# Performance work log

Hardware: AMD Instinct MI355X
Metric: run time of the kernel (lower is better)

The kernel has to match this reference:

```python
import jax, jax.numpy as jnp
import numpy as np

HIDDEN = 2304
HEADS = 16
THETA = 10000.0
LN_EPS = 1e-5


def setup_inputs() -> dict:
    key = jax.random.key(0)
    ks = jax.random.split(key, 6)
    d = HIDDEN
    init = lambda k, shape: jax.random.normal(k, shape, jnp.float32) * 0.02
    return {
        "x": jax.random.normal(ks[0], (4, 2048, d), jnp.float32),
        "wq": init(ks[1], (d, d)), "bq": jnp.zeros((d,), jnp.float32),
        "wk": init(ks[2], (d, d)), "bk": jnp.zeros((d,), jnp.float32),
        "wv": init(ks[3], (d, d)), "bv": jnp.zeros((d,), jnp.float32),
        "wo": init(ks[4], (d, d)), "bo": jnp.zeros((d,), jnp.float32),
        "ln_g": jnp.ones((d,), jnp.float32),
        "ln_b": jnp.zeros((d,), jnp.float32),
    }


def reference(x, wq, bq, wk, bk, wv, bv, wo, bo, ln_g, ln_b):
    b, s, d = x.shape
    H = HEADS
    Dh = d // H

    # qkv projections (nn.Linear: x @ W^T + b)
    q = jnp.einsum('bsd,ed->bse', x, wq) + bq
    k = jnp.einsum('bsd,ed->bse', x, wk) + bk
    v = jnp.einsum('bsd,ed->bse', x, wv) + bv

    # RoPE over the FULL hidden dim (d/2 pairs), as in the source
    pos = jnp.arange(s, dtype=jnp.float32)                    # (s,)
    scale = jnp.arange(0, d, 2, dtype=jnp.float32) / d        # (d/2,)
    omega = 1.0 / (THETA ** scale)                            # (d/2,)
    ang = pos[:, None] * omega[None, :]                       # (s, d/2)
    cos, sin = jnp.cos(ang), jnp.sin(ang)

    def rot(t):
        t2 = t.reshape(b, s, d // 2, 2)
        x0, x1 = t2[..., 0], t2[..., 1]
        return jnp.stack([cos * x0 - sin * x1, sin * x0 + cos * x1], axis=-1).reshape(b, s, d)

    q, k = rot(q), rot(k)

    # split heads -> (b, H, s, Dh)
    q = q.reshape(b, s, H, Dh).transpose(0, 2, 1, 3)
    k = k.reshape(b, s, H, Dh).transpose(0, 2, 1, 3)
    v = v.reshape(b, s, H, Dh).transpose(0, 2, 1, 3)

    # NOTE: faithful to source: einsum labels make this HEAD-mixing
    # attention at each position: logits shape (b, H, s, H)
    att_scale = 1.0 / (Dh ** 0.5)
    logits = jnp.einsum('bnhd,bmhd->bnhm', q, k) * att_scale
    w = jax.nn.softmax(logits, axis=-1)                       # (b,H,s,H)
    out = jnp.einsum('bnhm,bmhd->bnhd', w, v)                 # (b,H,s,Dh)

    out = out.transpose(0, 2, 1, 3).reshape(b, s, d)
    out = jnp.einsum('bsd,ed->bse', out, wo) + bo

    # residual + LayerNorm (dropout in eval mode -> identity)
    y = x + out
    mu = jnp.mean(y, axis=-1, keepdims=True)
    var = jnp.mean((y - mu) ** 2, axis=-1, keepdims=True)
    return (y - mu) * jax.lax.rsqrt(var + LN_EPS) * ln_g + ln_b
```

## Files before the change

### kernel.cpp

```cpp
#include <hip/hip_runtime.h>
#include <stdint.h>
#include <stddef.h>

#define D_HID 2304
#define NTOK  8192
#define NQKV  6912
#define WELEMS 5308416
#define SEQ_MASK 2047

typedef unsigned short u16;
typedef __bf16 bf16x8 __attribute__((ext_vector_type(8)));
typedef float  f32x16 __attribute__((ext_vector_type(16)));
typedef float  f32x4  __attribute__((ext_vector_type(4)));

__device__ __forceinline__ u16 f2bf(float f) {
    unsigned int u = __builtin_bit_cast(unsigned int, f);
    u += 0x7fffu + ((u >> 16) & 1u);
    return (u16)(u >> 16);
}
__device__ __forceinline__ float bf2f(u16 h) {
    unsigned int u = ((unsigned int)h) << 16;
    return __builtin_bit_cast(float, u);
}

__device__ __forceinline__ void gl2lds16(const void* g, void* l) {
    __builtin_amdgcn_global_load_lds(
        (const __attribute__((address_space(1))) void*)g,
        (__attribute__((address_space(3))) void*)l,
        16, 0, 0);
}

__global__ __launch_bounds__(256) void cvt_f32_bf16(
    const float* __restrict__ src, u16* __restrict__ dst)
{
    size_t i = ((size_t)blockIdx.x * 256 + threadIdx.x) * 4;
    float4 f = *(const float4*)(src + i);
    ushort4 o = make_ushort4(f2bf(f.x), f2bf(f.y), f2bf(f.z), f2bf(f.w));
    *(ushort4*)(dst + i) = o;
}

__global__ __launch_bounds__(256) void cvt_weights(
    const float* __restrict__ wq, const float* __restrict__ wk,
    const float* __restrict__ wv, const float* __restrict__ wo,
    u16* __restrict__ dst,
    const float* __restrict__ bq, const float* __restrict__ bk,
    const float* __restrict__ bv, float* __restrict__ bqkv)
{
    int i = blockIdx.x * 256 + threadIdx.x;
    if (i < NQKV)
        bqkv[i] = (i < 2304) ? bq[i] : (i < 4608) ? bk[i - 2304] : bv[i - 4608];
    size_t base = (size_t)i * 4;
    int r = (int)(base / WELEMS);
    const float* src = (r == 0) ? wq : (r == 1) ? wk : (r == 2) ? wv : wo;
    float4 f = *(const float4*)(src + (base - (size_t)r * WELEMS));
    ushort4 o = make_ushort4(f2bf(f.x), f2bf(f.y), f2bf(f.z), f2bf(f.w));
    *(ushort4*)(dst + base) = o;
}

__global__ __launch_bounds__(512, 2) void gemm256_bt(
    const u16* __restrict__ A, const u16* __restrict__ B,
    const float* __restrict__ bias, u16* __restrict__ Cout,
    int M, int N, int K)
{
    __shared__ __align__(16) u16 lds2[65536];

    const int tid  = threadIdx.x;
    const int lane = tid & 63;
    const int wave = tid >> 6;
    const int NT   = K >> 6;
    (void)M;

    const int chunk = gridDim.x >> 3;
    const int bid = (blockIdx.x & 7) * chunk + (blockIdx.x >> 3);
    const int num_bn = N >> 8;
    const int bm = bid / num_bn;
    const int bn = bid - bm * num_bn;

    const int srow = lane >> 3;
    const u16* __restrict__ Ast = A + (size_t)(bm * 256 + wave * 8 + srow) * K
                                    + ((lane & 7) ^ srow) * 8;
    const u16* __restrict__ Bst = B + (size_t)(bn * 256 + wave * 8 + srow) * K
                                    + ((lane & 7) ^ srow) * 8;
    const size_t row64  = (size_t)64 * K;
    const size_t row128 = (size_t)128 * K;
    const int ldsW = wave * 512;

#define STAGE(buf, hsel, tt) do {                                              \
    const u16* g_ = ((hsel) < 2 ? Ast : Bst)                                   \
                    + (((hsel) & 1) ? row128 : 0) + (size_t)(tt) * 64;         \
    u16* l_ = lds2 + (buf) * 32768 + (((hsel) < 2) ? 0 : 16384)                \
              + (((hsel) & 1) ? 8192 : 0) + ldsW;                              \
    gl2lds16(g_, l_);                                                          \
    gl2lds16(g_ + row64, l_ + 4096);                                           \
} while (0)

    const int l15 = lane & 15, l4 = lane >> 4;
    const int aBase = (wave >> 2) * 8192 + l15 * 64;
    const int bBase = 16384 + ((wave >> 1) & 1) * 8192
                      + ((wave & 1) * 64 + l15) * 64;
    const int s0 = ((l4    ) ^ (lane & 7)) * 8;
    const int s1 = ((l4 + 4) ^ (lane & 7)) * 8;

    f32x4 acc[8][4] = {};
    bf16x8 Bk0[4], Bk1[4], Aev[4], Aod[4];

    STAGE(0, 2, 0); STAGE(0, 3, 0); STAGE(0, 0, 0); STAGE(0, 1, 0);
    STAGE(1, 2, 1); STAGE(1, 3, 1); STAGE(1, 0, 1);
    asm volatile("s_waitcnt vmcnt(6)" ::: "memory");
    __builtin_amdgcn_s_barrier();
#pragma unroll
    for (int n = 0; n < 4; ++n)
        Bk0[n] = *(const bf16x8*)(lds2 + bBase + n * 1024 + s0);
#pragma unroll
    for (int mo = 0; mo < 4; ++mo)
        Aev[mo] = *(const bf16x8*)(lds2 + aBase + mo * 1024 + s0);

    for (int t = 0; t < NT; ++t) {
        const int cur = t & 1;
        const u16* lc = lds2 + cur * 32768;
        const u16* ln = lds2 + (cur ^ 1) * 32768;
        const bool st1 = (t + 1 < NT);
        const bool st2 = (t + 2 < NT);

#pragma unroll
        for (int n = 0; n < 4; ++n)
            Bk1[n] = *(const bf16x8*)(lc + bBase + n * 1024 + s1);
#pragma unroll
        for (int mo = 0; mo < 4; ++mo)
            Aod[mo] = *(const bf16x8*)(lc + aBase + (4 + mo) * 1024 + s0);
        if (st1) STAGE(cur ^ 1, 1, t + 1);
        __builtin_amdgcn_sched_barrier(0);
        __builtin_amdgcn_s_setprio(1);
#pragma unroll
        for (int mo = 0; mo < 4; ++mo)
#pragma unroll
            for (int n = 0; n < 4; ++n)
                acc[mo][n] = __builtin_amdgcn_mfma_f32_16x16x32_bf16(
                    Aev[mo], Bk0[n], acc[mo][n], 0, 0, 0);
        __builtin_amdgcn_s_setprio(0);
        __builtin_amdgcn_sched_barrier(0);
        __builtin_amdgcn_s_barrier();

#pragma unroll
        for (int mo = 0; mo < 4; ++mo)
            Aev[mo] = *(const bf16x8*)(lc + aBase + mo * 1024 + s1);
        if (st2) STAGE(cur, 2, t + 2);
        __builtin_amdgcn_sched_barrier(0);
        __builtin_amdgcn_s_setprio(1);
#pragma unroll
        for (int mo = 0; mo < 4; ++mo)
#pragma unroll
            for (int n = 0; n < 4; ++n)
                acc[4 + mo][n] = __builtin_amdgcn_mfma_f32_16x16x32_bf16(
                    Aod[mo], Bk0[n], acc[4 + mo][n], 0, 0, 0);
        __builtin_amdgcn_s_setprio(0);
        __builtin_amdgcn_sched_barrier(0);
        asm volatile("s_waitcnt lgkmcnt(0)" ::: "memory");
        __builtin_amdgcn_s_barrier();

#pragma unroll
        for (int mo = 0; mo < 4; ++mo)
            Aod[mo] = *(const bf16x8*)(lc + aBase + (4 + mo) * 1024 + s1);
        if (st2) STAGE(cur, 3, t + 2);
        if (st2)      asm volatile("s_waitcnt vmcnt(4)" ::: "memory");
        else if (st1) asm volatile("s_waitcnt vmcnt(0)" ::: "memory");
        if (st1) {
            __builtin_amdgcn_s_barrier();
#pragma unroll
            for (int n = 0; n < 4; ++n)
                Bk0[n] = *(const bf16x8*)(ln + bBase + n * 1024 + s0);
        }
        __builtin_amdgcn_sched_barrier(0);
        __builtin_amdgcn_s_setprio(1);
#pragma unroll
        for (int mo = 0; mo < 4; ++mo)
#pragma unroll
            for (int n = 0; n < 4; ++n)
                acc[mo][n] = __builtin_amdgcn_mfma_f32_16x16x32_bf16(
                    Aev[mo], Bk1[n], acc[mo][n], 0, 0, 0);
        __builtin_amdgcn_s_setprio(0);
        __builtin_amdgcn_sched_barrier(0);
        asm volatile("s_waitcnt lgkmcnt(0)" ::: "memory");
        __builtin_amdgcn_s_barrier();

        if (st2) STAGE(cur, 0, t + 2);
        if (st1) {
#pragma unroll
            for (int mo = 0; mo < 4; ++mo)
                Aev[mo] = *(const bf16x8*)(ln + aBase + mo * 1024 + s0);
        }
        __builtin_amdgcn_sched_barrier(0);
        __builtin_amdgcn_s_setprio(1);
#pragma unroll
        for (int mo = 0; mo < 4; ++mo)
#pragma unroll
            for (int n = 0; n < 4; ++n)
                acc[4 + mo][n] = __builtin_amdgcn_mfma_f32_16x16x32_bf16(
                    Aod[mo], Bk1[n], acc[4 + mo][n], 0, 0, 0);
        __builtin_amdgcn_s_setprio(0);
        __builtin_amdgcn_sched_barrier(0);
        asm volatile("s_waitcnt lgkmcnt(0)" ::: "memory");
        __builtin_amdgcn_s_barrier();
    }
#undef STAGE

    const int wm0 = (wave >> 2) * 128, wn0 = (wave & 3) * 64;
#pragma unroll
    for (int n = 0; n < 4; ++n) {
        const int gn = bn * 256 + wn0 + n * 16 + l15;
        const float bv = bias[gn];
#pragma unroll
        for (int m = 0; m < 8; ++m) {
            const int gm = bm * 256 + wm0 + m * 16 + l4 * 4;
#pragma unroll
            for (int j = 0; j < 4; ++j)
                Cout[(size_t)(gm + j) * N + gn] = f2bf(acc[m][n][j] + bv);
        }
    }
}

template<int MODE>
__global__ __launch_bounds__(256, 3) void gemm_bt(
    const u16* __restrict__ A, const u16* __restrict__ B,
    const float* __restrict__ bias, u16* __restrict__ Cout,
    const u16* __restrict__ resid, int M, int N, int K)
{
    __shared__ __align__(16) u16 As[128 * 64];
    __shared__ __align__(16) u16 Bs[128 * 64];

    const int tid  = threadIdx.x;
    const int lane = tid & 63;
    const int wave = tid >> 6;

    const int num_bn = N >> 7;
    const int rem = blockIdx.x % (num_bn << 3);
    const int bn  = rem >> 3;
    const int bm  = ((blockIdx.x / (num_bn << 3)) << 3) + (rem & 7);

    const int srow = tid >> 3;
    const int sc   = (tid & 7) ^ (srow & 7);
    const u16* Ag = A + (size_t)(bm * 128 + srow) * K + sc * 8;
    const u16* Bg = B + (size_t)(bn * 128 + srow) * K + sc * 8;
    const size_t row32 = (size_t)32 * K;
    u16* asd = As + wave * 512;
    u16* bsd = Bs + wave * 512;

    const int rl = lane & 31;
    const int h  = lane >> 5;
    const int swz = rl & 7;
    const int wm = (wave >> 1) * 64;
    const int wn = (wave & 1) * 64;

    f32x16 acc[2][2] = {};

    for (int kb = 0; kb < K; kb += 64) {
        __syncthreads();
#pragma unroll
        for (int r = 0; r < 4; ++r) {
            gl2lds16(Ag + kb + r * row32, asd + r * 2048);
            gl2lds16(Bg + kb + r * row32, bsd + r * 2048);
        }
        __syncthreads();

#pragma unroll
        for (int s = 0; s < 4; ++s) {
            const int ch = ((s * 2 + h) ^ swz) * 8;
            bf16x8 a0 = *(const bf16x8*)(As + (wm      + rl) * 64 + ch);
            bf16x8 a1 = *(const bf16x8*)(As + (wm + 32 + rl) * 64 + ch);
            bf16x8 b0 = *(const bf16x8*)(Bs + (wn      + rl) * 64 + ch);
            bf16x8 b1 = *(const bf16x8*)(Bs + (wn + 32 + rl) * 64 + ch);
            acc[0][0] = __builtin_amdgcn_mfma_f32_32x32x16_bf16(a0, b0, acc[0][0], 0, 0, 0);
            acc[0][1] = __builtin_amdgcn_mfma_f32_32x32x16_bf16(a0, b1, acc[0][1], 0, 0, 0);
            acc[1][0] = __builtin_amdgcn_mfma_f32_32x32x16_bf16(a1, b0, acc[1][0], 0, 0, 0);
            acc[1][1] = __builtin_amdgcn_mfma_f32_32x32x16_bf16(a1, b1, acc[1][1], 0, 0, 0);
        }
    }

#pragma unroll
    for (int mt = 0; mt < 2; ++mt) {
#pragma unroll
        for (int nt = 0; nt < 2; ++nt) {
            const int gn = bn * 128 + wn + nt * 32 + rl;
            const float bv = bias[gn];
#pragma unroll
            for (int reg = 0; reg < 16; ++reg) {
                const int gm = bm * 128 + wm + mt * 32 +
                               (reg & 3) + 8 * (reg >> 2) + 4 * h;
                const size_t idx = (size_t)gm * N + gn;
                float v = acc[mt][nt][reg] + bv;
                if constexpr (MODE == 1) v += bf2f(resid[idx]);
                Cout[idx] = f2bf(v);
            }
        }
    }
}

#define HROW 148
__global__ __launch_bounds__(256) void attn_headmix(
    const u16* __restrict__ QKV, u16* __restrict__ Aout)
{
    __shared__ __align__(16) float qs[16 * HROW];
    __shared__ __align__(16) float ks[16 * HROW];
    __shared__ __align__(16) float vs[16 * HROW];
    __shared__ __align__(16) float wsmT[256];

    const int tid = threadIdx.x;
    const int t   = blockIdx.x;
    const float fpos = (float)(t & SEQ_MASK);
    const u16* row = QKV + (size_t)t * NQKV;

    const float OMEGA_C = -2.0f * 13.287712379549449f / 2304.0f;
    const float INV2PI  = 0.15915494309189535f;

    for (int c = tid; c < 864; c += 256) {
        uint4 raw = *(const uint4*)(row + c * 8);
        float f[8];
        f[0] = bf2f(raw.x & 0xffff); f[1] = bf2f(raw.x >> 16);
        f[2] = bf2f(raw.y & 0xffff); f[3] = bf2f(raw.y >> 16);
        f[4] = bf2f(raw.z & 0xffff); f[5] = bf2f(raw.z >> 16);
        f[6] = bf2f(raw.w & 0xffff); f[7] = bf2f(raw.w >> 16);
        if (c < 576) {
            const int cc = (c < 288) ? c : c - 288;
            const int p0 = cc * 4;
#pragma unroll
            for (int jp = 0; jp < 4; ++jp) {
                float omega = exp2f((float)(p0 + jp) * OMEGA_C);
                float rr = fpos * omega * INV2PI;
                rr -= floorf(rr);
                float sn = __builtin_amdgcn_sinf(rr);
                float cs = __builtin_amdgcn_cosf(rr);
                float x0 = f[2 * jp], x1 = f[2 * jp + 1];
                f[2 * jp]     = cs * x0 - sn * x1;
                f[2 * jp + 1] = sn * x0 + cs * x1;
            }
            const int hr = cc / 18, col = (cc - hr * 18) * 8;
            float* dst = ((c < 288) ? qs : ks) + hr * HROW + col;
            *(float4*)(dst)     = make_float4(f[0], f[1], f[2], f[3]);
            *(float4*)(dst + 4) = make_float4(f[4], f[5], f[6], f[7]);
        } else {
            const int cv = c - 576;
            const int hr = cv / 18, col = (cv - hr * 18) * 8;
            float* dst = vs + hr * HROW + col;
            *(float4*)(dst)     = make_float4(f[0], f[1], f[2], f[3]);
            *(float4*)(dst + 4) = make_float4(f[4], f[5], f[6], f[7]);
        }
    }
    __syncthreads();

    const int n = tid >> 4, m = tid & 15;
    const float* qr = qs + n * HROW;
    const float* kr = ks + m * HROW;
    float s = 0.f;
#pragma unroll
    for (int d = 0; d < 144; d += 4) {
        float4 qv = *(const float4*)(qr + d);
        float4 kv = *(const float4*)(kr + d);
        s += qv.x * kv.x + qv.y * kv.y + qv.z * kv.z + qv.w * kv.w;
    }
    s *= (1.0f / 12.0f);

    float mx = s;
#pragma unroll
    for (int off = 8; off >= 1; off >>= 1) mx = fmaxf(mx, __shfl_xor(mx, off));
    float e = __expf(s - mx);
    float sum = e;
#pragma unroll
    for (int off = 8; off >= 1; off >>= 1) sum += __shfl_xor(sum, off);
    wsmT[m * 16 + n] = e / sum;
    __syncthreads();

    if (tid < 144) {
        const int col4 = tid % 36;
        const int nq   = tid / 36;
        const int oc   = col4 * 4;
        float4 a0 = {0,0,0,0}, a1 = {0,0,0,0}, a2 = {0,0,0,0}, a3 = {0,0,0,0};
#pragma unroll
        for (int mm = 0; mm < 16; ++mm) {
            float4 w4 = *(const float4*)(wsmT + mm * 16 + nq * 4);
            float4 v4 = *(const float4*)(vs + mm * HROW + oc);
            a0.x += w4.x * v4.x; a0.y += w4.x * v4.y; a0.z += w4.x * v4.z; a0.w += w4.x * v4.w;
            a1.x += w4.y * v4.x; a1.y += w4.y * v4.y; a1.z += w4.y * v4.z; a1.w += w4.y * v4.w;
            a2.x += w4.z * v4.x; a2.y += w4.z * v4.y; a2.z += w4.z * v4.z; a2.w += w4.z * v4.w;
            a3.x += w4.w * v4.x; a3.y += w4.w * v4.y; a3.z += w4.w * v4.z; a3.w += w4.w * v4.w;
        }
        u16* orow = Aout + (size_t)t * D_HID;
        float4 accs[4] = {a0, a1, a2, a3};
#pragma unroll
        for (int i = 0; i < 4; ++i) {
            const int nn = nq * 4 + i;
            ushort4 o = make_ushort4(f2bf(accs[i].x), f2bf(accs[i].y),
                                     f2bf(accs[i].z), f2bf(accs[i].w));
            *(ushort4*)(orow + nn * 144 + oc) = o;
        }
    }
}

__global__ __launch_bounds__(256) void ln_kernel(
    const u16* __restrict__ Y, const float* __restrict__ g,
    const float* __restrict__ b, float* __restrict__ out)
{
    const int tid  = threadIdx.x;
    const u16* y = Y + (size_t)blockIdx.x * D_HID;
    float v[9];
    float s = 0.f, s2 = 0.f;
#pragma unroll
    for (int r = 0; r < 9; ++r) {
        v[r] = bf2f(y[tid + r * 256]);
        s += v[r]; s2 += v[r] * v[r];
    }
#pragma unroll
    for (int off = 32; off >= 1; off >>= 1) {
        s  += __shfl_xor(s, off);
        s2 += __shfl_xor(s2, off);
    }
    __shared__ float red[8];
    const int wave = tid >> 6;
    if ((tid & 63) == 0) { red[wave] = s; red[4 + wave] = s2; }
    __syncthreads();
    s  = red[0] + red[1] + red[2] + red[3];
    s2 = red[4] + red[5] + red[6] + red[7];
    const float inv_n = 1.0f / 2304.0f;
    float mu  = s * inv_n;
    float var = fmaxf(s2 * inv_n - mu * mu, 0.f);
    float inv = rsqrtf(var + 1e-5f);
    float* orow = out + (size_t)blockIdx.x * D_HID;
#pragma unroll
    for (int r = 0; r < 9; ++r) {
        int c = tid + r * 256;
        orow[c] = (v[r] - mu) * inv * g[c] + b[c];
    }
}

extern "C" void kernel_launch(void* const* d_in, const int* in_sizes, int n_in,
                              void* d_out, int out_size, void* d_ws, size_t ws_size,
                              hipStream_t stream)
{
    const float* x   = (const float*)d_in[0];
    const float* wq  = (const float*)d_in[1];
    const float* bq  = (const float*)d_in[2];
    const float* wk  = (const float*)d_in[3];
    const float* bk  = (const float*)d_in[4];
    const float* wv  = (const float*)d_in[5];
    const float* bv  = (const float*)d_in[6];
    const float* wo  = (const float*)d_in[7];
    const float* bo  = (const float*)d_in[8];
    const float* lng = (const float*)d_in[9];
    const float* lnb = (const float*)d_in[10];

    char* ws = (char*)d_ws;
    size_t off = 0;
    auto alloc = [&](size_t bytes) {
        void* p = ws + off;
        off += (bytes + 255) & ~(size_t)255;
        return p;
    };
    u16*   xb   = (u16*)alloc((size_t)NTOK * D_HID * 2);
    u16*   wqkv = (u16*)alloc((size_t)(NQKV + D_HID) * D_HID * 2);
    u16*   wob  = wqkv + (size_t)NQKV * D_HID;
    float* bqkv = (float*)alloc((size_t)NQKV * 4);
    u16*   qkv  = (u16*)alloc((size_t)NTOK * NQKV * 2);
    u16*   aout = (u16*)alloc((size_t)NTOK * D_HID * 2);
    u16*   ybuf = qkv;

    cvt_f32_bf16<<<NTOK * D_HID / 1024, 256, 0, stream>>>(x, xb);
    cvt_weights<<<4 * WELEMS / 1024, 256, 0, stream>>>(wq, wk, wv, wo, wqkv,
                                                       bq, bk, bv, bqkv);
    gemm256_bt<<<(NTOK / 256) * (NQKV / 256), 512, 0, stream>>>(
        xb, wqkv, bqkv, qkv, NTOK, NQKV, D_HID);
    attn_headmix<<<NTOK, 256, 0, stream>>>(qkv, aout);
    gemm_bt<1><<<(D_HID / 128) * (NTOK / 128), 256, 0, stream>>>(
        aout, wob, bo, ybuf, xb, NTOK, D_HID, D_HID);
    ln_kernel<<<NTOK, 256, 0, stream>>>(ybuf, lng, lnb, (float*)d_out);
}
```

Baseline: 654.9 us.

## Precompute RoPE cos/sin table, reorder GEMM LDS loads, vectorize LayerNorm

Adds a kernel that precomputes a per-position cos/sin lookup table, so the attention kernel reads it instead of evaluating exp2/sin/cos for every token. The main QKV GEMM loop moves the Bk0 LDS reload into the later phase alongside the Aev loads, which removes one barrier and issues the global STAGE afterwards. LayerNorm now uses vectorized uint4/float4 loads and stores. Trade-offs: the table costs about 18MB of extra reads plus a launch, and the changed GEMM ordering shifts how loads overlap with MFMA work.

Result: no change. 653.5 us (-0.2%).

```diff
diff --git a/kernel.cpp b/kernel.cpp
--- a/kernel.cpp
+++ b/kernel.cpp
@@ -57,6 +57,22 @@
     *(ushort4*)(dst + base) = o;
 }
 
+__global__ __launch_bounds__(256) void rope_lut_k(float* __restrict__ lut)
+{
+    const float OMEGA_C = -2.0f * 13.287712379549449f / 2304.0f;
+    const float INV2PI  = 0.15915494309189535f;
+    const float fpos = (float)blockIdx.x;
+    float* row = lut + (size_t)blockIdx.x * 2304;
+    for (int p = threadIdx.x; p < 1152; p += 256) {
+        float omega = exp2f((float)p * OMEGA_C);
+        float rr = fpos * omega * INV2PI;
+        rr -= floorf(rr);
+        float sn = __builtin_amdgcn_sinf(rr);
+        float cs = __builtin_amdgcn_cosf(rr);
+        *(float2*)(row + 2 * p) = make_float2(cs, sn);
+    }
+}
+
 __global__ __launch_bounds__(512, 2) void gemm256_bt(
     const u16* __restrict__ A, const u16* __restrict__ B,
     const float* __restrict__ bias, u16* __restrict__ Cout,
@@ -164,12 +180,6 @@
         if (st2) STAGE(cur, 3, t + 2);
         if (st2)      asm volatile("s_waitcnt vmcnt(4)" ::: "memory");
         else if (st1) asm volatile("s_waitcnt vmcnt(0)" ::: "memory");
-        if (st1) {
-            __builtin_amdgcn_s_barrier();
-#pragma unroll
-            for (int n = 0; n < 4; ++n)
-                Bk0[n] = *(const bf16x8*)(ln + bBase + n * 1024 + s0);
-        }
         __builtin_amdgcn_sched_barrier(0);
         __builtin_amdgcn_s_setprio(1);
 #pragma unroll
@@ -183,12 +193,15 @@
         asm volatile("s_waitcnt lgkmcnt(0)" ::: "memory");
         __builtin_amdgcn_s_barrier();
 
-        if (st2) STAGE(cur, 0, t + 2);
         if (st1) {
+#pragma unroll
+            for (int n = 0; n < 4; ++n)
+                Bk0[n] = *(const bf16x8*)(ln + bBase + n * 1024 + s0);
 #pragma unroll
             for (int mo = 0; mo < 4; ++mo)
                 Aev[mo] = *(const bf16x8*)(ln + aBase + mo * 1024 + s0);
         }
+        if (st2) STAGE(cur, 0, t + 2);
         __builtin_amdgcn_sched_barrier(0);
         __builtin_amdgcn_s_setprio(1);
 #pragma unroll
@@ -297,7 +310,8 @@
 
 #define HROW 148
 __global__ __launch_bounds__(256) void attn_headmix(
-    const u16* __restrict__ QKV, u16* __restrict__ Aout)
+    const u16* __restrict__ QKV, const float* __restrict__ lut,
+    u16* __restrict__ Aout)
 {
     __shared__ __align__(16) float qs[16 * HROW];
     __shared__ __align__(16) float ks[16 * HROW];
@@ -306,11 +320,8 @@
 
     const int tid = threadIdx.x;
     const int t   = blockIdx.x;
-    const float fpos = (float)(t & SEQ_MASK);
     const u16* row = QKV + (size_t)t * NQKV;
-
-    const float OMEGA_C = -2.0f * 13.287712379549449f / 2304.0f;
-    const float INV2PI  = 0.15915494309189535f;
+    const float* lutrow = lut + (size_t)(t & SEQ_MASK) * 2304;
 
     for (int c = tid; c < 864; c += 256) {
         uint4 raw = *(const uint4*)(row + c * 8);
@@ -321,18 +332,13 @@
         f[6] = bf2f(raw.w & 0xffff); f[7] = bf2f(raw.w >> 16);
         if (c < 576) {
             const int cc = (c < 288) ? c : c - 288;
-            const int p0 = cc * 4;
-#pragma unroll
-            for (int jp = 0; jp < 4; ++jp) {
-                float omega = exp2f((float)(p0 + jp) * OMEGA_C);
-                float rr = fpos * omega * INV2PI;
-                rr -= floorf(rr);
-                float sn = __builtin_amdgcn_sinf(rr);
-                float cs = __builtin_amdgcn_cosf(rr);
-                float x0 = f[2 * jp], x1 = f[2 * jp + 1];
-                f[2 * jp]     = cs * x0 - sn * x1;
-                f[2 * jp + 1] = sn * x0 + cs * x1;
-            }
+            const float4 t0 = *(const float4*)(lutrow + cc * 8);
+            const float4 t1 = *(const float4*)(lutrow + cc * 8 + 4);
+            float x0, x1;
+            x0 = f[0]; x1 = f[1]; f[0] = t0.x * x0 - t0.y * x1; f[1] = t0.y * x0 + t0.x * x1;
+            x0 = f[2]; x1 = f[3]; f[2] = t0.z * x0 - t0.w * x1; f[3] = t0.w * x0 + t0.z * x1;
+            x0 = f[4]; x1 = f[5]; f[4] = t1.x * x0 - t1.y * x1; f[5] = t1.y * x0 + t1.x * x1;
+            x0 = f[6]; x1 = f[7]; f[6] = t1.z * x0 - t1.w * x1; f[7] = t1.w * x0 + t1.z * x1;
             const int hr = cc / 18, col = (cc - hr * 18) * 8;
             float* dst = ((c < 288) ? qs : ks) + hr * HROW + col;
             *(float4*)(dst)     = make_float4(f[0], f[1], f[2], f[3]);
@@ -401,13 +407,17 @@
 {
     const int tid  = threadIdx.x;
     const u16* y = Y + (size_t)blockIdx.x * D_HID;
+    uint4 raw = *(const uint4*)(y + tid * 8);
+    u16 extra = y[2048 + tid];
     float v[9];
+    v[0] = bf2f(raw.x & 0xffff); v[1] = bf2f(raw.x >> 16);
+    v[2] = bf2f(raw.y & 0xffff); v[3] = bf2f(raw.y >> 16);
+    v[4] = bf2f(raw.z & 0xffff); v[5] = bf2f(raw.z >> 16);
+    v[6] = bf2f(raw.w & 0xffff); v[7] = bf2f(raw.w >> 16);
+    v[8] = bf2f(extra);
     float s = 0.f, s2 = 0.f;
 #pragma unroll
-    for (int r = 0; r < 9; ++r) {
-        v[r] = bf2f(y[tid + r * 256]);
-        s += v[r]; s2 += v[r] * v[r];
-    }
+    for (int r = 0; r < 9; ++r) { s += v[r]; s2 += v[r] * v[r]; }
 #pragma unroll
     for (int off = 32; off >= 1; off >>= 1) {
         s  += __shfl_xor(s, off);
@@ -424,11 +434,22 @@
     float var = fmaxf(s2 * inv_n - mu * mu, 0.f);
     float inv = rsqrtf(var + 1e-5f);
     float* orow = out + (size_t)blockIdx.x * D_HID;
-#pragma unroll
-    for (int r = 0; r < 9; ++r) {
-        int c = tid + r * 256;
-        orow[c] = (v[r] - mu) * inv * g[c] + b[c];
-    }
+    float4 g0 = *(const float4*)(g + tid * 8);
+    float4 g1 = *(const float4*)(g + tid * 8 + 4);
+    float4 b0 = *(const float4*)(b + tid * 8);
+    float4 b1 = *(const float4*)(b + tid * 8 + 4);
+    float4 o0, o1;
+    o0.x = (v[0] - mu) * inv * g0.x + b0.x;
+    o0.y = (v[1] - mu) * inv * g0.y + b0.y;
+    o0.z = (v[2] - mu) * inv * g0.z + b0.z;
+    o0.w = (v[3] - mu) * inv * g0.w + b0.w;
+    o1.x = (v[4] - mu) * inv * g1.x + b1.x;
+    o1.y = (v[5] - mu) * inv * g1.y + b1.y;
+    o1.z = (v[6] - mu) * inv * g1.z + b1.z;
+    o1.w = (v[7] - mu) * inv * g1.w + b1.w;
+    *(float4*)(orow + tid * 8)     = o0;
+    *(float4*)(orow + tid * 8 + 4) = o1;
+    orow[2048 + tid] = (v[8] - mu) * inv * g[2048 + tid] + b[2048 + tid];
 }
 
 extern "C" void kernel_launch(void* const* d_in, const int* in_sizes, int n_in,
@@ -460,14 +481,16 @@
     float* bqkv = (float*)alloc((size_t)NQKV * 4);
     u16*   qkv  = (u16*)alloc((size_t)NTOK * NQKV * 2);
     u16*   aout = (u16*)alloc((size_t)NTOK * D_HID * 2);
+    float* lutw = (float*)alloc((size_t)2048 * 2304 * 4);
     u16*   ybuf = qkv;
 
+    rope_lut_k<<<2048, 256, 0, stream>>>(lutw);
     cvt_f32_bf16<<<NTOK * D_HID / 1024, 256, 0, stream>>>(x, xb);
     cvt_weights<<<4 * WELEMS / 1024, 256, 0, stream>>>(wq, wk, wv, wo, wqkv,
                                                        bq, bk, bv, bqkv);
     gemm256_bt<<<(NTOK / 256) * (NQKV / 256), 512, 0, stream>>>(
         xb, wqkv, bqkv, qkv, NTOK, NQKV, D_HID);
-    attn_headmix<<<NTOK, 256, 0, stream>>>(qkv, aout);
+    attn_headmix<<<NTOK, 256, 0, stream>>>(qkv, lutw, aout);
     gemm_bt<1><<<(D_HID / 128) * (NTOK / 128), 256, 0, stream>>>(
         aout, wob, bo, ybuf, xb, NTOK, D_HID, D_HID);
     ln_kernel<<<NTOK, 256, 0, stream>>>(ybuf, lng, lnb, (float*)d_out);
```
